# Kernel tuning notes

Measured on AMD Instinct MI355X. Metric: run time of the kernel, lower is better.

## Reference

```python
import jax, jax.numpy as jnp
import numpy as np

DIM = 5120
HEADS = 40
HEAD_DIM = DIM // HEADS
EPS = 1e-6


def rms_norm(x, w, eps=EPS):
    var = jnp.mean(jnp.square(x), axis=-1, keepdims=True)
    return x * jax.lax.rsqrt(var + eps) * w


def apply_rotary(x, freqs_cos, freqs_sin):
    # x: [B, L, H, D]; freqs: [1, L, 1, D] (broadcastable)
    x_even = x[..., 0::2]
    x_odd = x[..., 1::2]
    cos_e = freqs_cos[..., 0::2]
    sin_o = freqs_sin[..., 1::2]
    out_even = x_even * cos_e - x_odd * sin_o
    out_odd = x_even * sin_o + x_odd * cos_e
    # interleave back: [..., D//2, 2] -> [..., D]
    return jnp.stack([out_even, out_odd], axis=-1).reshape(x.shape)


def setup_inputs() -> dict:
    key = jax.random.key(0)
    ks = jax.random.split(key, 8)
    B, L = 1, 2048
    scale_in = 1.0 / np.sqrt(DIM)
    return {
        "hidden_states": jax.random.normal(ks[0], (B, L, DIM), jnp.float32),
        "freqs_cos": jax.random.normal(ks[1], (1, L, 1, HEAD_DIM), jnp.float32),
        "freqs_sin": jax.random.normal(ks[2], (1, L, 1, HEAD_DIM), jnp.float32),
        "W_qkv": jax.random.normal(ks[3], (DIM, 3 * DIM), jnp.float32) * scale_in,
        "b_qkv": jnp.zeros((3 * DIM,), jnp.float32),
        "w_norm_q": jnp.ones((DIM,), jnp.float32),
        "w_norm_k": jnp.ones((DIM,), jnp.float32),
        "W_out": jax.random.normal(ks[4], (DIM, DIM), jnp.float32) * scale_in,
        "b_out": jnp.zeros((DIM,), jnp.float32),
    }


def reference(hidden_states, freqs_cos, freqs_sin, W_qkv, b_qkv,
              w_norm_q, w_norm_k, W_out, b_out):
    B, L, D = hidden_states.shape
    qkv = hidden_states @ W_qkv + b_qkv                     # [B, L, 3D]
    q, k, v = jnp.split(qkv, 3, axis=-1)
    q = rms_norm(q, w_norm_q)                               # norm over full dim=5120
    k = rms_norm(k, w_norm_k)
    q = q.reshape(B, L, HEADS, HEAD_DIM)
    k = k.reshape(B, L, HEADS, HEAD_DIM)
    v = v.reshape(B, L, HEADS, HEAD_DIM)
    q = apply_rotary(q, freqs_cos, freqs_sin)
    k = apply_rotary(k, freqs_cos, freqs_sin)
    scale = 1.0 / np.sqrt(HEAD_DIM)
    scores = jnp.einsum("bqhd,bkhd->bhqk", q, k) * scale    # [B, H, L, L]
    attn = jax.nn.softmax(scores, axis=-1)
    out = jnp.einsum("bhqk,bkhd->bqhd", attn, v)            # [B, L, H, D]
    out = out.reshape(B, L, D)
    return out @ W_out + b_out
```

## Files before the change

### kernel.cpp

```cpp
#include <hip/hip_runtime.h>
#include <cstdint>
#include <cstddef>

#define L_C   2048
#define DIMC  5120
#define HD    128
#define NHEADS 40

typedef __bf16 bf16_t;
typedef __bf16 bf16x8 __attribute__((ext_vector_type(8)));
typedef __bf16 bf16x4 __attribute__((ext_vector_type(4)));
typedef float  f32x4  __attribute__((ext_vector_type(4)));

#define MFMA16(A,B,C) __builtin_amdgcn_mfma_f32_16x16x32_bf16((A),(B),(C),0,0,0)
#define BARRIER() __builtin_amdgcn_s_barrier()
#define LGKM0()  asm volatile("s_waitcnt lgkmcnt(0)" ::: "memory")
#define VMCNT0() asm volatile("s_waitcnt vmcnt(0)" ::: "memory")
#define VMCNT4() asm volatile("s_waitcnt vmcnt(4)" ::: "memory")
#define VMCNT6() asm volatile("s_waitcnt vmcnt(6)" ::: "memory")
#define VMCNT8() asm volatile("s_waitcnt vmcnt(8)" ::: "memory")

__device__ __forceinline__ void gload16(const void* g, void* l) {
  __builtin_amdgcn_global_load_lds(
      (__attribute__((address_space(1))) void*)(void*)g,
      (__attribute__((address_space(3))) void*)l, 16, 0, 0);
}

__global__ __launch_bounds__(256) void f32_to_bf16(const float* __restrict__ in,
                                                   bf16_t* __restrict__ out, size_t n8) {
  size_t i = (size_t)blockIdx.x * blockDim.x + threadIdx.x;
  size_t stride = (size_t)gridDim.x * blockDim.x;
  for (; i < n8; i += stride) {
    f32x4 a = *(const f32x4*)(in + i * 8);
    f32x4 b = *(const f32x4*)(in + i * 8 + 4);
    bf16x8 o;
#pragma unroll
    for (int j = 0; j < 4; ++j) { o[j] = (bf16_t)a[j]; o[4 + j] = (bf16_t)b[j]; }
    *(bf16x8*)(out + i * 8) = o;
  }
}

__global__ __launch_bounds__(256) void wtrans(const float* __restrict__ W,
                                              bf16_t* __restrict__ Wt, int K, int N) {
  __shared__ bf16_t t[64 * 68];
  const int k0 = blockIdx.x * 64, n0 = blockIdx.y * 64, tid = threadIdx.x;
  const int tn = tid & 15, tk = tid >> 4;
  f32x4 v[4];
#pragma unroll
  for (int jj = 0; jj < 4; ++jj)
    v[jj] = *(const f32x4*)(W + (size_t)(k0 + 4 * tk + jj) * N + n0 + 4 * tn);
#pragma unroll
  for (int j = 0; j < 4; ++j) {
    bf16x4 o;
#pragma unroll
    for (int jj = 0; jj < 4; ++jj) o[jj] = (bf16_t)v[jj][j];
    *(bf16x4*)&t[(4 * tn + j) * 68 + 4 * tk] = o;
  }
  __syncthreads();
#pragma unroll
  for (int i = 0; i < 2; ++i) {
    int c = i * 256 + tid, rn = c >> 3, ck = (c & 7) * 8;
    bf16x8 o = *(const bf16x8*)&t[rn * 68 + ck];
    *(bf16x8*)(Wt + (size_t)(n0 + rn) * K + k0 + ck) = o;
  }
}

__global__ __launch_bounds__(256) void v_trans(const bf16_t* __restrict__ qkv,
                                               bf16_t* __restrict__ Vt) {
  __shared__ bf16_t t[128 * 68];
  const int l0 = blockIdx.x * 64, h = blockIdx.y, tid = threadIdx.x;
  const int td = tid & 31, tl = tid >> 5;
#pragma unroll
  for (int it = 0; it < 2; ++it) {
    const int lq = tl + it * 8;
    bf16x4 v[4];
#pragma unroll
    for (int jj = 0; jj < 4; ++jj)
      v[jj] = *(const bf16x4*)(qkv + (size_t)(l0 + 4 * lq + jj) * (3 * DIMC) +
                               2 * DIMC + h * HD + 4 * td);
#pragma unroll
    for (int j = 0; j < 4; ++j) {
      bf16x4 o;
#pragma unroll
      for (int jj = 0; jj < 4; ++jj) o[jj] = v[jj][j];
      *(bf16x4*)&t[(4 * td + j) * 68 + 4 * lq] = o;
    }
  }
  __syncthreads();
#pragma unroll
  for (int i = 0; i < 4; ++i) {
    int c = i * 256 + tid, d = c >> 3, cl = (c & 7) * 8;
    bf16x8 o = *(const bf16x8*)&t[d * 68 + cl];
    *(bf16x8*)(Vt + ((size_t)h * HD + d) * L_C + l0 + cl) = o;
  }
}

template <int OUT_BF16, int K>
__global__ __launch_bounds__(512, 1) void gemm8(const bf16_t* __restrict__ A,
                                                const bf16_t* __restrict__ Bt,
                                                const float* __restrict__ bias,
                                                bf16_t* __restrict__ Cb,
                                                float* __restrict__ Cf,
                                                int M, int N) {
  __shared__ __align__(16) char smem[131072];
  const int tid = threadIdx.x;
  const int wid = tid >> 6, lane = tid & 63;
  const int g = lane >> 4, r = lane & 15;
  const int wm = wid >> 2, wn = wid & 3;
  const int nb = gridDim.x * gridDim.y;
  const int bid = blockIdx.y * gridDim.x + blockIdx.x;
  const int swz = (bid & 7) * (nb >> 3) + (bid >> 3);
  const int bm = swz % gridDim.x, bn = swz / gridDim.x;
  const int row0 = bm * 256, col0 = bn * 256;

  auto stageA = [&](int buf, int half, int kt) {
#pragma unroll
    for (int i = 0; i < 2; ++i) {
      const int idx = i * 512 + tid;
      const int rl = idx >> 3, c = idx & 7;
      gload16(A + (size_t)(row0 + half * 128 + rl) * K + kt * 64 + ((c ^ (rl & 7)) << 3),
              smem + buf * 65536 + half * 16384 + (i * 512 + wid * 64) * 16);
    }
  };
  auto stageB = [&](int buf, int half, int kt) {
#pragma unroll
    for (int i = 0; i < 2; ++i) {
      const int idx = i * 512 + tid;
      const int rl = idx >> 3, c = idx & 7;
      gload16(Bt + (size_t)(col0 + half * 128 + rl) * K + kt * 64 + ((c ^ (rl & 7)) << 3),
              smem + buf * 65536 + 32768 + half * 16384 + (i * 512 + wid * 64) * 16);
    }
  };
  auto ldA = [&](int buf, int mi, int kk) {
    const int rh = mi * 16 + r;
    return *(const bf16x8*)(smem + buf * 65536 + wm * 16384 + rh * 128 +
                            (((kk * 4 + g) ^ (r & 7)) << 4));
  };
  auto ldB = [&](int buf, int ni, int kk) {
    const int rh = (wn & 1) * 64 + ni * 16 + r;
    return *(const bf16x8*)(smem + buf * 65536 + 32768 + (wn >> 1) * 16384 + rh * 128 +
                            (((kk * 4 + g) ^ (r & 7)) << 4));
  };

  f32x4 acc[8][4] = {};
  bf16x8 af[4][2], bfr[4][2];
  constexpr int nk = K / 64;

  stageA(0, 0, 0); stageA(0, 1, 0); stageB(0, 0, 0); stageB(0, 1, 0);
  stageA(1, 0, 1); stageA(1, 1, 1); stageB(1, 0, 1); stageB(1, 1, 1);
  VMCNT8();
  BARRIER();

  for (int t = 0; t < nk; t += 2) {
    const bool first = (t == 0);
    const bool pf2 = (t + 2 < nk);
    const bool pf3 = (t + 3 < nk);
#pragma unroll
    for (int i = 0; i < 4; ++i)
#pragma unroll
      for (int kk = 0; kk < 2; ++kk) af[i][kk] = ldA(0, i, kk);
#pragma unroll
    for (int j = 0; j < 2; ++j)
#pragma unroll
      for (int kk = 0; kk < 2; ++kk) bfr[j][kk] = ldB(0, j, kk);
    if (!first) stageA(1, 1, t + 1);
    BARRIER(); LGKM0();
    __builtin_amdgcn_s_setprio(1);
#pragma unroll
    for (int i = 0; i < 4; ++i)
#pragma unroll
      for (int j = 0; j < 2; ++j)
#pragma unroll
        for (int kk = 0; kk < 2; ++kk) acc[i][j] = MFMA16(af[i][kk], bfr[j][kk], acc[i][j]);
    __builtin_amdgcn_s_setprio(0);
    BARRIER();
#pragma unroll
    for (int j = 0; j < 2; ++j)
#pragma unroll
      for (int kk = 0; kk < 2; ++kk) bfr[2 + j][kk] = ldB(0, 2 + j, kk);
    BARRIER(); LGKM0();
    __builtin_amdgcn_s_setprio(1);
#pragma unroll
    for (int i = 0; i < 4; ++i)
#pragma unroll
      for (int j = 0; j < 2; ++j)
#pragma unroll
        for (int kk = 0; kk < 2; ++kk) acc[i][2 + j] = MFMA16(af[i][kk], bfr[2 + j][kk], acc[i][2 + j]);
    __builtin_amdgcn_s_setprio(0);
    BARRIER();
#pragma unroll
    for (int i = 0; i < 4; ++i)
#pragma unroll
      for (int kk = 0; kk < 2; ++kk) af[i][kk] = ldA(0, 4 + i, kk);
    if (pf2) stageB(0, 0, t + 2);
    BARRIER(); LGKM0();
    __builtin_amdgcn_s_setprio(1);
#pragma unroll
    for (int i = 0; i < 4; ++i)
#pragma unroll
      for (int j = 0; j < 2; ++j)
#pragma unroll
        for (int kk = 0; kk < 2; ++kk) acc[4 + i][2 + j] = MFMA16(af[i][kk], bfr[2 + j][kk], acc[4 + i][2 + j]);
    __builtin_amdgcn_s_setprio(0);
    BARRIER();
    if (pf2) stageA(0, 0, t + 2);
    BARRIER();
    __builtin_amdgcn_s_setprio(1);
#pragma unroll
    for (int i = 0; i < 4; ++i)
#pragma unroll
      for (int j = 0; j < 2; ++j)
#pragma unroll
        for (int kk = 0; kk < 2; ++kk) acc[4 + i][j] = MFMA16(af[i][kk], bfr[j][kk], acc[4 + i][j]);
    __builtin_amdgcn_s_setprio(0);
    if (pf2) { VMCNT4(); } else { VMCNT0(); }
    BARRIER();
#pragma unroll
    for (int i = 0; i < 4; ++i)
#pragma unroll
      for (int kk = 0; kk < 2; ++kk) af[i][kk] = ldA(1, i, kk);
#pragma unroll
    for (int j = 0; j < 2; ++j)
#pragma unroll
      for (int kk = 0; kk < 2; ++kk) bfr[j][kk] = ldB(1, j, kk);
    if (pf2) stageB(0, 1, t + 2);
    BARRIER(); LGKM0();
    __builtin_amdgcn_s_setprio(1);
#pragma unroll
    for (int i = 0; i < 4; ++i)
#pragma unroll
      for (int j = 0; j < 2; ++j)
#pragma unroll
        for (int kk = 0; kk < 2; ++kk) acc[i][j] = MFMA16(af[i][kk], bfr[j][kk], acc[i][j]);
    __builtin_amdgcn_s_setprio(0);
    BARRIER();
#pragma unroll
    for (int j = 0; j < 2; ++j)
#pragma unroll
      for (int kk = 0; kk < 2; ++kk) bfr[2 + j][kk] = ldB(1, 2 + j, kk);
    if (pf2) stageA(0, 1, t + 2);
    BARRIER(); LGKM0();
    __builtin_amdgcn_s_setprio(1);
#pragma unroll
    for (int i = 0; i < 4; ++i)
#pragma unroll
      for (int j = 0; j < 2; ++j)
#pragma unroll
        for (int kk = 0; kk < 2; ++kk) acc[i][2 + j] = MFMA16(af[i][kk], bfr[2 + j][kk], acc[i][2 + j]);
    __builtin_amdgcn_s_setprio(0);
    BARRIER();
#pragma unroll
    for (int i = 0; i < 4; ++i)
#pragma unroll
      for (int kk = 0; kk < 2; ++kk) af[i][kk] = ldA(1, 4 + i, kk);
    if (pf3) stageB(1, 0, t + 3);
    BARRIER(); LGKM0();
    __builtin_amdgcn_s_setprio(1);
#pragma unroll
    for (int i = 0; i < 4; ++i)
#pragma unroll
      for (int j = 0; j < 2; ++j)
#pragma unroll
        for (int kk = 0; kk < 2; ++kk) acc[4 + i][2 + j] = MFMA16(af[i][kk], bfr[2 + j][kk], acc[4 + i][2 + j]);
    __builtin_amdgcn_s_setprio(0);
    BARRIER();
    if (pf3) { stageB(1, 1, t + 3); stageA(1, 0, t + 3); }
    BARRIER();
    __builtin_amdgcn_s_setprio(1);
#pragma unroll
    for (int i = 0; i < 4; ++i)
#pragma unroll
      for (int j = 0; j < 2; ++j)
#pragma unroll
        for (int kk = 0; kk < 2; ++kk) acc[4 + i][j] = MFMA16(af[i][kk], bfr[j][kk], acc[4 + i][j]);
    __builtin_amdgcn_s_setprio(0);
    if (pf2) { VMCNT6(); } else { VMCNT0(); }
    BARRIER();
  }

#pragma unroll
  for (int mi = 0; mi < 8; ++mi)
#pragma unroll
    for (int ni = 0; ni < 4; ++ni)
#pragma unroll
      for (int p = 0; p < 4; ++p) {
        const int rr = row0 + wm * 128 + mi * 16 + 4 * g + p;
        const int cc = col0 + wn * 64 + ni * 16 + r;
        const float v = acc[mi][ni][p] + bias[cc];
        if (OUT_BF16) Cb[(size_t)rr * N + cc] = (bf16_t)v;
        else          Cf[(size_t)rr * N + cc] = v;
      }
}

__global__ __launch_bounds__(256) void norm_rope(const bf16_t* __restrict__ qkv,
                                                 const float* __restrict__ wq,
                                                 const float* __restrict__ wk,
                                                 const float* __restrict__ fcos,
                                                 const float* __restrict__ fsin,
                                                 bf16_t* __restrict__ Qo,
                                                 bf16_t* __restrict__ Ko) {
  __shared__ bf16_t qs[DIMC], ks_[DIMC];
  const int l = blockIdx.x, tid = threadIdx.x;
  const bf16_t* row = qkv + (size_t)l * (3 * DIMC);
  float sq = 0.f, sk = 0.f;
  for (int i = tid; i < DIMC / 8; i += 256) {
    bf16x8 a = *(const bf16x8*)(row + i * 8);
    bf16x8 b = *(const bf16x8*)(row + DIMC + i * 8);
    *(bf16x8*)&qs[i * 8] = a;
    *(bf16x8*)&ks_[i * 8] = b;
#pragma unroll
    for (int j = 0; j < 8; ++j) {
      float x = (float)a[j]; sq += x * x;
      float y = (float)b[j]; sk += y * y;
    }
  }
#pragma unroll
  for (int off = 32; off; off >>= 1) {
    sq += __shfl_xor(sq, off, 64);
    sk += __shfl_xor(sk, off, 64);
  }
  __shared__ float red[2][4];
  const int wid = tid >> 6, lane = tid & 63;
  if (!lane) { red[0][wid] = sq; red[1][wid] = sk; }
  __syncthreads();
  sq = red[0][0] + red[0][1] + red[0][2] + red[0][3];
  sk = red[1][0] + red[1][1] + red[1][2] + red[1][3];
  const float rq = rsqrtf(sq * (1.f / DIMC) + 1e-6f);
  const float rk = rsqrtf(sk * (1.f / DIMC) + 1e-6f);
  for (int i = tid; i < DIMC / 8; i += 256) {
    const int j0 = i * 8, h = j0 >> 7, d0 = j0 & 127;
    bf16x8 a = *(const bf16x8*)&qs[j0];
    bf16x8 b = *(const bf16x8*)&ks_[j0];
    f32x4 cA = *(const f32x4*)(fcos + (size_t)l * HD + d0);
    f32x4 cB = *(const f32x4*)(fcos + (size_t)l * HD + d0 + 4);
    f32x4 sA = *(const f32x4*)(fsin + (size_t)l * HD + d0);
    f32x4 sB = *(const f32x4*)(fsin + (size_t)l * HD + d0 + 4);
    f32x4 wqA = *(const f32x4*)(wq + j0), wqB = *(const f32x4*)(wq + j0 + 4);
    f32x4 wkA = *(const f32x4*)(wk + j0), wkB = *(const f32x4*)(wk + j0 + 4);
    float cc[8], ss[8], qn[8], kn[8];
#pragma unroll
    for (int j = 0; j < 4; ++j) {
      cc[j] = cA[j]; cc[4 + j] = cB[j];
      ss[j] = sA[j]; ss[4 + j] = sB[j];
      qn[j] = (float)a[j] * rq * wqA[j];
      qn[4 + j] = (float)a[4 + j] * rq * wqB[j];
      kn[j] = (float)b[j] * rk * wkA[j];
      kn[4 + j] = (float)b[4 + j] * rk * wkB[j];
    }
    bf16x8 oq, ok;
#pragma unroll
    for (int p = 0; p < 4; ++p) {
      const float c = cc[2 * p], s = ss[2 * p + 1];
      oq[2 * p]     = (bf16_t)(qn[2 * p] * c - qn[2 * p + 1] * s);
      oq[2 * p + 1] = (bf16_t)(qn[2 * p] * s + qn[2 * p + 1] * c);
      ok[2 * p]     = (bf16_t)(kn[2 * p] * c - kn[2 * p + 1] * s);
      ok[2 * p + 1] = (bf16_t)(kn[2 * p] * s + kn[2 * p + 1] * c);
    }
    *(bf16x8*)(Qo + ((size_t)h * L_C + l) * HD + d0) = oq;
    *(bf16x8*)(Ko + ((size_t)h * L_C + l) * HD + d0) = ok;
  }
}

__global__ __launch_bounds__(256, 2) void attn(const bf16_t* __restrict__ Q,
                                               const bf16_t* __restrict__ Kg,
                                               const bf16_t* __restrict__ Vt,
                                               bf16_t* __restrict__ O) {
  __shared__ bf16_t k_lds[64 * HD];
  __shared__ bf16_t v_lds[HD * 64];
  __shared__ bf16_t p_lds[4][2][16 * 72];
  const int tid = threadIdx.x, wid = tid >> 6, lane = tid & 63;
  const int g = lane >> 4, r = lane & 15;
  const int bid = blockIdx.x;
  const int grp = bid & 7, inner = bid >> 3;
  const int h = (inner >> 4) * 8 + grp;
  const int q0 = (inner & 15) * 128 + wid * 32;
  bf16x8 qf[2][4];
#pragma unroll
  for (int rg = 0; rg < 2; ++rg) {
    const bf16_t* qrow = Q + ((size_t)h * L_C + q0 + rg * 16 + r) * HD;
#pragma unroll
    for (int ks = 0; ks < 4; ++ks) qf[rg][ks] = *(const bf16x8*)(qrow + ks * 32 + g * 8);
  }
  f32x4 oacc[2][8] = {};
  float m_i[2][4], l_i[2][4];
#pragma unroll
  for (int rg = 0; rg < 2; ++rg)
#pragma unroll
    for (int p = 0; p < 4; ++p) { m_i[rg][p] = -1e30f; l_i[rg][p] = 0.f; }
  const float scale = 0.08838834764831845f;

  bf16x8 kreg[4], vreg[4];
  auto load_kv = [&](int kv0) {
#pragma unroll
    for (int i = 0; i < 4; ++i) {
      const int c = i * 256 + tid;
      const int krow = c >> 4, kcb = c & 15;
      kreg[i] = *(const bf16x8*)(Kg + ((size_t)h * L_C + kv0 + krow) * HD + kcb * 8);
      const int vrow = c >> 3, vcb = c & 7;
      vreg[i] = *(const bf16x8*)(Vt + ((size_t)h * HD + vrow) * L_C + kv0 + vcb * 8);
    }
  };
  load_kv(0);

  for (int kv0 = 0; kv0 < L_C; kv0 += 64) {
    __syncthreads();
#pragma unroll
    for (int i = 0; i < 4; ++i) {
      const int c = i * 256 + tid;
      const int krow = c >> 4, kcb = c & 15;
      *(bf16x8*)((char*)k_lds + krow * 256 + ((kcb * 16) ^ ((krow & 7) << 4))) = kreg[i];
      const int vrow = c >> 3, vcb = c & 7;
      *(bf16x8*)((char*)v_lds + vrow * 128 + ((vcb * 16) ^ ((vrow & 7) << 4))) = vreg[i];
    }
    if (kv0 + 64 < L_C) load_kv(kv0 + 64);
    __syncthreads();

    float pv[2][4][4];
    __builtin_amdgcn_s_setprio(1);
#pragma unroll
    for (int nf = 0; nf < 4; ++nf) {
      f32x4 s0 = {0.f, 0.f, 0.f, 0.f}, s1 = {0.f, 0.f, 0.f, 0.f};
      const int key = nf * 16 + r;
#pragma unroll
      for (int ks = 0; ks < 4; ++ks) {
        bf16x8 kf = *(const bf16x8*)((const char*)k_lds + key * 256 +
                                     ((ks * 64 + g * 16) ^ ((key & 7) << 4)));
        s0 = MFMA16(qf[0][ks], kf, s0);
        s1 = MFMA16(qf[1][ks], kf, s1);
      }
#pragma unroll
      for (int p = 0; p < 4; ++p) { pv[0][nf][p] = s0[p] * scale; pv[1][nf][p] = s1[p] * scale; }
    }
    __builtin_amdgcn_s_setprio(0);
#pragma unroll
    for (int rg = 0; rg < 2; ++rg) {
      float mnew[4];
#pragma unroll
      for (int p = 0; p < 4; ++p)
        mnew[p] = fmaxf(fmaxf(pv[rg][0][p], pv[rg][1][p]), fmaxf(pv[rg][2][p], pv[rg][3][p]));
#pragma unroll
      for (int m = 1; m < 16; m <<= 1)
#pragma unroll
        for (int p = 0; p < 4; ++p) mnew[p] = fmaxf(mnew[p], __shfl_xor(mnew[p], m, 64));
      float alpha[4], rsum[4];
#pragma unroll
      for (int p = 0; p < 4; ++p) {
        const float mi = fmaxf(m_i[rg][p], mnew[p]);
        alpha[p] = __expf(m_i[rg][p] - mi);
        m_i[rg][p] = mi;
        rsum[p] = 0.f;
      }
#pragma unroll
      for (int nf = 0; nf < 4; ++nf)
#pragma unroll
        for (int p = 0; p < 4; ++p) {
          pv[rg][nf][p] = __expf(pv[rg][nf][p] - m_i[rg][p]);
          rsum[p] += pv[rg][nf][p];
        }
#pragma unroll
      for (int nf = 0; nf < 4; ++nf)
#pragma unroll
        for (int p = 0; p < 4; ++p)
          p_lds[wid][rg][(4 * g + p) * 72 + nf * 16 + r] = (bf16_t)pv[rg][nf][p];
#pragma unroll
      for (int m = 1; m < 16; m <<= 1)
#pragma unroll
        for (int p = 0; p < 4; ++p) rsum[p] += __shfl_xor(rsum[p], m, 64);
#pragma unroll
      for (int p = 0; p < 4; ++p) l_i[rg][p] = l_i[rg][p] * alpha[p] + rsum[p];
#pragma unroll
      for (int nf = 0; nf < 8; ++nf)
#pragma unroll
        for (int p = 0; p < 4; ++p) oacc[rg][nf][p] *= alpha[p];
    }
    bf16x8 pf0[2], pf1[2];
#pragma unroll
    for (int rg = 0; rg < 2; ++rg) {
      pf0[rg] = *(const bf16x8*)&p_lds[wid][rg][r * 72 + 8 * g];
      pf1[rg] = *(const bf16x8*)&p_lds[wid][rg][r * 72 + 32 + 8 * g];
    }
    __builtin_amdgcn_s_setprio(1);
#pragma unroll
    for (int nf = 0; nf < 8; ++nf) {
      const int d = nf * 16 + r;
      bf16x8 vf0 = *(const bf16x8*)((const char*)v_lds + d * 128 +
                                    ((g * 16) ^ ((d & 7) << 4)));
      bf16x8 vf1 = *(const bf16x8*)((const char*)v_lds + d * 128 +
                                    ((64 + g * 16) ^ ((d & 7) << 4)));
#pragma unroll
      for (int rg = 0; rg < 2; ++rg) {
        oacc[rg][nf] = MFMA16(pf0[rg], vf0, oacc[rg][nf]);
        oacc[rg][nf] = MFMA16(pf1[rg], vf1, oacc[rg][nf]);
      }
    }
    __builtin_amdgcn_s_setprio(0);
  }
#pragma unroll
  for (int rg = 0; rg < 2; ++rg)
#pragma unroll
    for (int p = 0; p < 4; ++p) {
      const float inv = 1.f / l_i[rg][p];
      const int rowg = q0 + rg * 16 + 4 * g + p;
#pragma unroll
      for (int nf = 0; nf < 8; ++nf) {
        const int d = nf * 16 + r;
        O[(size_t)rowg * DIMC + h * HD + d] = (bf16_t)(oacc[rg][nf][p] * inv);
      }
    }
}

extern "C" void kernel_launch(void* const* d_in, const int* in_sizes, int n_in,
                              void* d_out, int out_size, void* d_ws, size_t ws_size,
                              hipStream_t stream) {
  const float* hidden = (const float*)d_in[0];
  const float* fcos   = (const float*)d_in[1];
  const float* fsin   = (const float*)d_in[2];
  const float* Wqkv   = (const float*)d_in[3];
  const float* bqkv   = (const float*)d_in[4];
  const float* wnq    = (const float*)d_in[5];
  const float* wnk    = (const float*)d_in[6];
  const float* Wout   = (const float*)d_in[7];
  const float* bout   = (const float*)d_in[8];
  float* out = (float*)d_out;

  char* ws = (char*)d_ws;
  size_t off = 0;
  auto alloc = [&](size_t bytes) {
    void* p = ws + off;
    off += (bytes + 255) & ~(size_t)255;
    return p;
  };
  bf16_t* X   = (bf16_t*)alloc((size_t)L_C * DIMC * 2);
  bf16_t* WQT = (bf16_t*)alloc((size_t)3 * DIMC * DIMC * 2);
  bf16_t* WOT = (bf16_t*)alloc((size_t)DIMC * DIMC * 2);
  bf16_t* QKV = (bf16_t*)alloc((size_t)L_C * 3 * DIMC * 2);
  bf16_t* Qb  = (bf16_t*)alloc((size_t)L_C * DIMC * 2);
  bf16_t* Kb  = (bf16_t*)alloc((size_t)L_C * DIMC * 2);
  bf16_t* VT  = (bf16_t*)alloc((size_t)L_C * DIMC * 2);
  bf16_t* Ob  = X;

  f32_to_bf16<<<2048, 256, 0, stream>>>(hidden, X, (size_t)L_C * DIMC / 8);
  wtrans<<<dim3(DIMC / 64, 3 * DIMC / 64), 256, 0, stream>>>(Wqkv, WQT, DIMC, 3 * DIMC);
  wtrans<<<dim3(DIMC / 64, DIMC / 64), 256, 0, stream>>>(Wout, WOT, DIMC, DIMC);
  gemm8<1, DIMC><<<dim3(L_C / 256, 3 * DIMC / 256), 512, 0, stream>>>(
      X, WQT, bqkv, QKV, nullptr, L_C, 3 * DIMC);
  norm_rope<<<L_C, 256, 0, stream>>>(QKV, wnq, wnk, fcos, fsin, Qb, Kb);
  v_trans<<<dim3(L_C / 64, NHEADS), 256, 0, stream>>>(QKV, VT);
  attn<<<(L_C / 128) * NHEADS, 256, 0, stream>>>(Qb, Kb, VT, Ob);
  gemm8<0, DIMC><<<dim3(L_C / 256, DIMC / 256), 512, 0, stream>>>(
      Ob, WOT, bout, nullptr, out, L_C, DIMC);
}
```

Baseline: 777.0 us.

## Split-K the output projection GEMM and skip rescaling in attention softmax

The output projection GEMM is split along K into two halves. Each half writes fp32 partial results into the reused QKV weight workspace, and a new reduction kernel adds the two partials plus the bias. The aim is to raise the block count from 160 toward filling the 256 CUs, at the cost of extra fp32 traffic and one more launch. Separately, the attention softmax now works in the exp2 domain with the log2e factor folded into the scale. It also applies the lazy-rescaling trick, which only rescales the accumulator and running sum when the running max grows by more than 8, cutting ALU work per tile.

```diff
diff --git a/kernel.cpp b/kernel.cpp
--- a/kernel.cpp
+++ b/kernel.cpp
@@ -95,30 +95,37 @@
   }
 }
 
-template <int OUT_BF16, int K>
+template <int OUTMODE, int K, int SPLITK>
 __global__ __launch_bounds__(512, 1) void gemm8(const bf16_t* __restrict__ A,
                                                 const bf16_t* __restrict__ Bt,
                                                 const float* __restrict__ bias,
                                                 bf16_t* __restrict__ Cb,
                                                 float* __restrict__ Cf,
-                                                int M, int N) {
+                                                int M, int N, int ldk) {
   __shared__ __align__(16) char smem[131072];
   const int tid = threadIdx.x;
   const int wid = tid >> 6, lane = tid & 63;
   const int g = lane >> 4, r = lane & 15;
   const int wm = wid >> 2, wn = wid & 3;
-  const int nb = gridDim.x * gridDim.y;
-  const int bid = blockIdx.y * gridDim.x + blockIdx.x;
+  const int gx = gridDim.x, gy = gridDim.y;
+  const int nb = gx * gy * (SPLITK > 1 ? gridDim.z : 1);
+  const int bid = ((SPLITK > 1 ? blockIdx.z : 0) * gy + blockIdx.y) * gx + blockIdx.x;
   const int swz = (bid & 7) * (nb >> 3) + (bid >> 3);
-  const int bm = swz % gridDim.x, bn = swz / gridDim.x;
+  const int bm = swz % gx;
+  const int rest = swz / gx;
+  const int bn = rest % gy;
+  const int ks = (SPLITK > 1) ? rest / gy : 0;
   const int row0 = bm * 256, col0 = bn * 256;
+  const bf16_t* Ap = A + (size_t)ks * K;
+  const bf16_t* Bp = Bt + (size_t)ks * K;
+  float* Cp = Cf + (size_t)ks * M * N;
 
   auto stageA = [&](int buf, int half, int kt) {
 #pragma unroll
     for (int i = 0; i < 2; ++i) {
       const int idx = i * 512 + tid;
       const int rl = idx >> 3, c = idx & 7;
-      gload16(A + (size_t)(row0 + half * 128 + rl) * K + kt * 64 + ((c ^ (rl & 7)) << 3),
+      gload16(Ap + (size_t)(row0 + half * 128 + rl) * ldk + kt * 64 + ((c ^ (rl & 7)) << 3),
               smem + buf * 65536 + half * 16384 + (i * 512 + wid * 64) * 16);
     }
   };
@@ -127,7 +134,7 @@
     for (int i = 0; i < 2; ++i) {
       const int idx = i * 512 + tid;
       const int rl = idx >> 3, c = idx & 7;
-      gload16(Bt + (size_t)(col0 + half * 128 + rl) * K + kt * 64 + ((c ^ (rl & 7)) << 3),
+      gload16(Bp + (size_t)(col0 + half * 128 + rl) * ldk + kt * 64 + ((c ^ (rl & 7)) << 3),
               smem + buf * 65536 + 32768 + half * 16384 + (i * 512 + wid * 64) * 16);
     }
   };
@@ -286,10 +293,26 @@
       for (int p = 0; p < 4; ++p) {
         const int rr = row0 + wm * 128 + mi * 16 + 4 * g + p;
         const int cc = col0 + wn * 64 + ni * 16 + r;
-        const float v = acc[mi][ni][p] + bias[cc];
-        if (OUT_BF16) Cb[(size_t)rr * N + cc] = (bf16_t)v;
-        else          Cf[(size_t)rr * N + cc] = v;
+        if (OUTMODE == 1) Cb[(size_t)rr * N + cc] = (bf16_t)(acc[mi][ni][p] + bias[cc]);
+        else              Cp[(size_t)rr * N + cc] = acc[mi][ni][p];
       }
+}
+
+__global__ __launch_bounds__(256) void reduce2(const float* __restrict__ part,
+                                               const float* __restrict__ bias,
+                                               float* __restrict__ out) {
+  const size_t MN = (size_t)L_C * DIMC;
+  size_t i = (size_t)blockIdx.x * blockDim.x + threadIdx.x;
+  const size_t stride = (size_t)gridDim.x * blockDim.x;
+  for (; i < MN / 4; i += stride) {
+    f32x4 a = *(const f32x4*)(part + i * 4);
+    f32x4 b = *(const f32x4*)(part + MN + i * 4);
+    f32x4 bi = *(const f32x4*)(bias + (i * 4) % DIMC);
+    f32x4 o;
+#pragma unroll
+    for (int j = 0; j < 4; ++j) o[j] = a[j] + b[j] + bi[j];
+    *(f32x4*)(out + i * 4) = o;
+  }
 }
 
 __global__ __launch_bounds__(256) void norm_rope(const bf16_t* __restrict__ qkv,
@@ -387,7 +410,7 @@
   for (int rg = 0; rg < 2; ++rg)
 #pragma unroll
     for (int p = 0; p < 4; ++p) { m_i[rg][p] = -1e30f; l_i[rg][p] = 0.f; }
-  const float scale = 0.08838834764831845f;
+  const float scale2 = 0.08838834764831845f * 1.4426950408889634f;
 
   bf16x8 kreg[4], vreg[4];
   auto load_kv = [&](int kv0) {
@@ -429,7 +452,7 @@
         s1 = MFMA16(qf[1][ks], kf, s1);
       }
 #pragma unroll
-      for (int p = 0; p < 4; ++p) { pv[0][nf][p] = s0[p] * scale; pv[1][nf][p] = s1[p] * scale; }
+      for (int p = 0; p < 4; ++p) { pv[0][nf][p] = s0[p] * scale2; pv[1][nf][p] = s1[p] * scale2; }
     }
     __builtin_amdgcn_s_setprio(0);
 #pragma unroll
@@ -442,19 +465,29 @@
       for (int m = 1; m < 16; m <<= 1)
 #pragma unroll
         for (int p = 0; p < 4; ++p) mnew[p] = fmaxf(mnew[p], __shfl_xor(mnew[p], m, 64));
-      float alpha[4], rsum[4];
-#pragma unroll
-      for (int p = 0; p < 4; ++p) {
-        const float mi = fmaxf(m_i[rg][p], mnew[p]);
-        alpha[p] = __expf(m_i[rg][p] - mi);
-        m_i[rg][p] = mi;
-        rsum[p] = 0.f;
+      bool grow = false;
+#pragma unroll
+      for (int p = 0; p < 4; ++p) grow = grow || (mnew[p] > m_i[rg][p] + 8.f);
+      if (__any(grow)) {
+        float al[4];
+#pragma unroll
+        for (int p = 0; p < 4; ++p) {
+          const float mi = fmaxf(m_i[rg][p], mnew[p]);
+          al[p] = exp2f(m_i[rg][p] - mi);
+          m_i[rg][p] = mi;
+          l_i[rg][p] *= al[p];
+        }
+#pragma unroll
+        for (int nf = 0; nf < 8; ++nf)
+#pragma unroll
+          for (int p = 0; p < 4; ++p) oacc[rg][nf][p] *= al[p];
       }
+      float rsum[4] = {0.f, 0.f, 0.f, 0.f};
 #pragma unroll
       for (int nf = 0; nf < 4; ++nf)
 #pragma unroll
         for (int p = 0; p < 4; ++p) {
-          pv[rg][nf][p] = __expf(pv[rg][nf][p] - m_i[rg][p]);
+          pv[rg][nf][p] = exp2f(pv[rg][nf][p] - m_i[rg][p]);
           rsum[p] += pv[rg][nf][p];
         }
 #pragma unroll
@@ -467,11 +500,7 @@
 #pragma unroll
         for (int p = 0; p < 4; ++p) rsum[p] += __shfl_xor(rsum[p], m, 64);
 #pragma unroll
-      for (int p = 0; p < 4; ++p) l_i[rg][p] = l_i[rg][p] * alpha[p] + rsum[p];
-#pragma unroll
-      for (int nf = 0; nf < 8; ++nf)
-#pragma unroll
-        for (int p = 0; p < 4; ++p) oacc[rg][nf][p] *= alpha[p];
+      for (int p = 0; p < 4; ++p) l_i[rg][p] += rsum[p];
     }
     bf16x8 pf0[2], pf1[2];
 #pragma unroll
@@ -538,15 +567,17 @@
   bf16_t* Kb  = (bf16_t*)alloc((size_t)L_C * DIMC * 2);
   bf16_t* VT  = (bf16_t*)alloc((size_t)L_C * DIMC * 2);
   bf16_t* Ob  = X;
+  float*  part = (float*)WQT;
 
   f32_to_bf16<<<2048, 256, 0, stream>>>(hidden, X, (size_t)L_C * DIMC / 8);
   wtrans<<<dim3(DIMC / 64, 3 * DIMC / 64), 256, 0, stream>>>(Wqkv, WQT, DIMC, 3 * DIMC);
   wtrans<<<dim3(DIMC / 64, DIMC / 64), 256, 0, stream>>>(Wout, WOT, DIMC, DIMC);
-  gemm8<1, DIMC><<<dim3(L_C / 256, 3 * DIMC / 256), 512, 0, stream>>>(
-      X, WQT, bqkv, QKV, nullptr, L_C, 3 * DIMC);
+  gemm8<1, DIMC, 1><<<dim3(L_C / 256, 3 * DIMC / 256), 512, 0, stream>>>(
+      X, WQT, bqkv, QKV, nullptr, L_C, 3 * DIMC, DIMC);
   norm_rope<<<L_C, 256, 0, stream>>>(QKV, wnq, wnk, fcos, fsin, Qb, Kb);
   v_trans<<<dim3(L_C / 64, NHEADS), 256, 0, stream>>>(QKV, VT);
   attn<<<(L_C / 128) * NHEADS, 256, 0, stream>>>(Qb, Kb, VT, Ob);
-  gemm8<0, DIMC><<<dim3(L_C / 256, DIMC / 256), 512, 0, stream>>>(
-      Ob, WOT, bout, nullptr, out, L_C, DIMC);
-}
+  gemm8<2, DIMC / 2, 2><<<dim3(L_C / 256, DIMC / 256, 2), 512, 0, stream>>>(
+      Ob, WOT, nullptr, nullptr, part, L_C, DIMC, DIMC);
+  reduce2<<<2048, 256, 0, stream>>>(part, bout, out);
+}
```

New measurement: 832.0 us. +7.1%, slower.
